# Kernel tuning notes

Measured on AMD Instinct MI355X. Metric: run time of the kernel, lower is better.

The kernel has to match this reference:

```python
import jax, jax.numpy as jnp
import numpy as np

BATCH, SEQ, HIDDEN = 2, 4096, 4096
HEADS, HEAD_DIM, BLOCK = 32, 128, 256
LAYER_IDX, N_LAYERS = 1, 32
EPS = 1e-5


def setup_inputs() -> dict:
    key = jax.random.key(0)
    ks = jax.random.split(key, 5)
    s = 0.02
    return {
        "hidden_states": jax.random.normal(ks[0], (BATCH, SEQ, HIDDEN), jnp.float32),
        "qkv_w": jax.random.normal(ks[1], (3 * HEADS * HEAD_DIM, HIDDEN), jnp.float32) * s,
        "out_w": jax.random.normal(ks[2], (HIDDEN, HEADS * HEAD_DIM), jnp.float32) * s,
        "gate_w": jax.random.normal(ks[3], (HEADS * HEAD_DIM, HIDDEN), jnp.float32) * s,
        "norm_w": jnp.ones((HEADS * HEAD_DIM,), jnp.float32),
    }


def _decays():
    # slope_rate: (h,1,1)
    base = 1.0 / 2.0 ** (8.0 / HEADS)
    exponent = jnp.arange(HEADS, dtype=jnp.float32) + 1.0
    factor = 1.0 - LAYER_IDX / (N_LAYERS - 1 + 1e-5) + 1e-5
    slope = (base ** exponent * factor)[:, None, None]
    r = jnp.arange(BLOCK, dtype=jnp.float32) + 1.0
    q_decay = jnp.exp(-slope * r[:, None])                 # (h, block, 1)
    k_decay = jnp.exp(-slope * (BLOCK - r)[:, None])       # (h, block, 1)
    diff = r[:, None] - r[None, :]                         # (block, block): i - j
    diag = slope[None] * diff[None, None]                  # (1, h, block, block)
    diag = jnp.where(diag >= 0, -diag, -jnp.inf)
    diag_decay = jnp.exp(diag)                             # causal intra-block decay
    block_decay = jnp.exp(-slope * BLOCK)                  # (h,1,1)
    return q_decay, k_decay, diag_decay, block_decay


def reference(hidden_states, qkv_w, out_w, gate_w, norm_w):
    b, s, _ = hidden_states.shape
    h, d, bs = HEADS, HEAD_DIM, BLOCK
    nb = s // bs
    q_decay, k_decay, diag_decay, block_decay = _decays()

    # qkv projection + silu, split per-head into q,k,v
    qkv = jax.nn.silu(hidden_states @ qkv_w.T)             # (b,s,3hd)
    qkv = qkv.reshape(b, s, h, 3, d)
    q = jnp.moveaxis(qkv[:, :, :, 0], 2, 1)                # (b,h,s,d)
    k = jnp.moveaxis(qkv[:, :, :, 1], 2, 1)
    v = jnp.moveaxis(qkv[:, :, :, 2], 2, 1)

    # split sequence into blocks, scan leading axis = block index
    def to_blocks(x):
        return jnp.moveaxis(x.reshape(b, h, nb, bs, d), 2, 0)  # (nb,b,h,bs,d)

    qb, kb, vb = to_blocks(q), to_blocks(k), to_blocks(v)

    def step(kv, blk):
        cq, ck, cv = blk
        # intra-block quadratic attention with causal decay
        scores = jnp.einsum('bhnd,bhmd->bhnm', cq, ck) * diag_decay
        intra = jnp.einsum('bhnm,bhmd->bhnd', scores, cv)
        # inter-block via decayed recurrent state kv: (b,h,d,d)
        inter = jnp.einsum('bhnd,bhde->bhne', cq * q_decay, kv)
        kv_next = kv * block_decay + jnp.einsum('bhnd,bhne->bhde', ck * k_decay, cv)
        return kv_next, intra + inter

    kv0 = jnp.zeros((b, h, d, d), hidden_states.dtype)
    _, out_blocks = jax.lax.scan(step, kv0, (qb, kb, vb))  # (nb,b,h,bs,d)

    attn = jnp.moveaxis(out_blocks, 0, 2)                  # (b,h,nb,bs,d)
    attn = attn.reshape(b, h, s, d).transpose(0, 2, 1, 3).reshape(b, s, h * d)

    # RMSNorm (fp32 accumulation, as MixtralRMSNorm)
    xf = attn.astype(jnp.float32)
    xf = xf * jax.lax.rsqrt(jnp.mean(xf * xf, axis=-1, keepdims=True) + EPS)
    normed = norm_w * xf.astype(attn.dtype)

    gate = jax.nn.sigmoid(hidden_states @ gate_w.T)
    return (gate * normed) @ out_w.T
```

## Files before the change

kernel.cpp:

```cpp
#include <hip/hip_runtime.h>

typedef unsigned short u16;
typedef __attribute__((ext_vector_type(4))) float f32x4;
typedef __attribute__((ext_vector_type(8))) __bf16 bf16x8;

#define SEQ   4096
#define HID   4096
#define HID3  12288

__device__ __forceinline__ float bf2f(u16 u){
  union { unsigned int i; float f; } v; v.i = ((unsigned int)u) << 16; return v.f;
}
__device__ __forceinline__ u16 f2bf(float f){
  union { float f; unsigned int i; } v; v.f = f;
  unsigned int r = (v.i + 0x7FFFu + ((v.i >> 16) & 1u)) >> 16;
  return (u16)r;
}
__device__ __forceinline__ float slope_of(int h){
  const float factor = 1.0f - 1.0f/(31.0f + 1e-5f) + 1e-5f;
  return exp2f(-0.25f * (float)(h + 1)) * factor;
}
__device__ __forceinline__ bf16x8 ld_bf8(const u16* p){
  return __builtin_bit_cast(bf16x8, *(const uint4*)p);
}
__device__ __forceinline__ void gload_lds16(const u16* g, u16* l){
  __builtin_amdgcn_global_load_lds((const __attribute__((address_space(1))) void*)g,
                                   (__attribute__((address_space(3))) void*)l, 16, 0, 0);
}

#define CVT_B0 33554432L
#define CVT_B1 83886080L
#define CVT_B2 100663296L
#define CVT_B3 117440512L
__global__ __launch_bounds__(256) void cvt4_kernel(const float* __restrict__ s0,
                                                   const float* __restrict__ s1,
                                                   const float* __restrict__ s2,
                                                   const float* __restrict__ s3,
                                                   u16* __restrict__ dst){
  long i = ((long)blockIdx.x * 256 + threadIdx.x) * 4;
  long stride = (long)gridDim.x * 1024;
  for (; i < CVT_B3; i += stride){
    const float* src;
    long off;
    if (i < CVT_B0){ src = s0; off = i; }
    else if (i < CVT_B1){ src = s1; off = i - CVT_B0; }
    else if (i < CVT_B2){ src = s2; off = i - CVT_B1; }
    else { src = s3; off = i - CVT_B2; }
    float4 v = *(const float4*)(src + off);
    ushort4 o;
    o.x = f2bf(v.x); o.y = f2bf(v.y); o.z = f2bf(v.z); o.w = f2bf(v.w);
    *(ushort4*)(dst + i) = o;
  }
}

template<int EPI>
__global__ __launch_bounds__(512) void gemm256(
    const u16* __restrict__ A, const u16* __restrict__ B, void* __restrict__ C,
    const u16* __restrict__ Aux, const float* __restrict__ Rs,
    const float* __restrict__ Nw, int M, int N, int K)
{
  __shared__ u16 ring[5][16384];
  const int t = threadIdx.x;
  const int w = t >> 6, l = t & 63, lr = l & 15, lk = l >> 4;
  const int mw = w >> 2, nw = w & 3;
  const int nbn = N >> 8;
  int nwg = gridDim.x;
  int bid = blockIdx.x;
  int bswz = (bid & 7) * (nwg >> 3) + (bid >> 3);
  int bm = bswz / nbn, bn = bswz % nbn;
  const u16* Abase = A + (long)(bm * 256) * K;
  const u16* Bbase = B + (long)(bn * 256) * K;
  const int NT = K >> 6;

  int sr[2], sku[2];
#pragma unroll
  for (int i = 0; i < 2; ++i){
    int dr = i * 64 + (t >> 3);
    int ul = (t & 7) ^ (dr & 7);
    sr[i]  = 2 * dr + (ul >> 2);
    sku[i] = ul & 3;
  }
  int offA[8], offB[4];
#pragma unroll
  for (int fn = 0; fn < 8; ++fn){
    int row = mw * 128 + fn * 16 + lr;
    offA[fn] = (row >> 1) * 64 + (((((row & 1) << 2) + lk) ^ ((row >> 1) & 7)) << 3);
  }
#pragma unroll
  for (int fe = 0; fe < 4; ++fe){
    int row = nw * 64 + fe * 16 + lr;
    offB[fe] = (row >> 1) * 64 + (((((row & 1) << 2) + lk) ^ ((row >> 1) & 7)) << 3);
  }

  auto stageA = [&](int kt, int c, int slot, int i){
    gload_lds16(Abase + (long)sr[i] * K + kt * 64 + c * 32 + sku[i] * 8,
                &ring[slot][i * 4096 + w * 512]);
  };
  auto stageB = [&](int kt, int c, int slot, int i){
    gload_lds16(Bbase + (long)sr[i] * K + kt * 64 + c * 32 + sku[i] * 8,
                &ring[slot][8192 + i * 4096 + w * 512]);
  };

  f32x4 acc[8][4] = {};

  stageA(0,0,0,0); stageA(0,0,0,1); stageB(0,0,0,0); stageB(0,0,0,1);
  stageA(0,1,1,0); stageA(0,1,1,1); stageB(0,1,1,0); stageB(0,1,1,1);
  if (1 < NT){ stageA(1,0,2,0); stageA(1,0,2,1); stageB(1,0,2,0); stageB(1,0,2,1); }
  asm volatile("s_waitcnt vmcnt(4)" ::: "memory");
  __builtin_amdgcn_s_barrier();

  int sa = 0;
  for (int p = 0; p < NT; ++p){
    int sb = sa + 1; if (sb >= 5) sb -= 5;
    int sx = sa + 3; if (sx >= 5) sx -= 5;
    int sy = sa + 4; if (sy >= 5) sy -= 5;
    const u16* Aa = &ring[sa][0];
    const u16* Ab = &ring[sb][0];
    const u16* Ba = &ring[sa][8192];
    const u16* Bb = &ring[sb][8192];
    bf16x8 bh0[4], bh1[4], afc0[8], afc1[8];

#pragma unroll
    for (int fe = 0; fe < 4; ++fe) bh0[fe] = ld_bf8(Ba + offB[fe]);
#pragma unroll
    for (int fn = 0; fn < 4; ++fn) afc0[fn] = ld_bf8(Aa + offA[fn]);
#pragma unroll
    for (int fn = 4; fn < 8; ++fn) afc0[fn] = ld_bf8(Aa + offA[fn]);
    if (p + 1 < NT){ stageA(p+1, 1, sx, 0); stageA(p+1, 1, sx, 1); }
    asm volatile("s_waitcnt lgkmcnt(4)" ::: "memory");
    __builtin_amdgcn_sched_barrier(0);
    __builtin_amdgcn_s_setprio(1);
#pragma unroll
    for (int fn = 0; fn < 4; ++fn)
#pragma unroll
      for (int fe = 0; fe < 4; ++fe)
        acc[fn][fe] = __builtin_amdgcn_mfma_f32_16x16x32_bf16(afc0[fn], bh0[fe], acc[fn][fe], 0, 0, 0);
    __builtin_amdgcn_s_setprio(0);

#pragma unroll
    for (int fe = 0; fe < 4; ++fe) bh1[fe] = ld_bf8(Bb + offB[fe]);
#pragma unroll
    for (int fn = 0; fn < 4; ++fn) afc1[fn] = ld_bf8(Ab + offA[fn]);
    if (p + 1 < NT){ stageB(p+1, 1, sx, 0); stageB(p+1, 1, sx, 1); }
    asm volatile("s_waitcnt lgkmcnt(8)" ::: "memory");
    __builtin_amdgcn_sched_barrier(0);
    __builtin_amdgcn_s_setprio(1);
#pragma unroll
    for (int fn = 4; fn < 8; ++fn)
#pragma unroll
      for (int fe = 0; fe < 4; ++fe)
        acc[fn][fe] = __builtin_amdgcn_mfma_f32_16x16x32_bf16(afc0[fn], bh0[fe], acc[fn][fe], 0, 0, 0);
    __builtin_amdgcn_s_setprio(0);

#pragma unroll
    for (int fn = 4; fn < 8; ++fn) afc1[fn] = ld_bf8(Ab + offA[fn]);
    if (p + 2 < NT){ stageA(p+2, 0, sy, 0); stageA(p+2, 0, sy, 1); }
    asm volatile("s_waitcnt lgkmcnt(4)" ::: "memory");
    __builtin_amdgcn_sched_barrier(0);
    __builtin_amdgcn_s_setprio(1);
#pragma unroll
    for (int fn = 0; fn < 4; ++fn)
#pragma unroll
      for (int fe = 0; fe < 4; ++fe)
        acc[fn][fe] = __builtin_amdgcn_mfma_f32_16x16x32_bf16(afc1[fn], bh1[fe], acc[fn][fe], 0, 0, 0);
    __builtin_amdgcn_s_setprio(0);

    if (p + 2 < NT){ stageB(p+2, 0, sy, 0); stageB(p+2, 0, sy, 1); }
    asm volatile("s_waitcnt lgkmcnt(0)" ::: "memory");
    __builtin_amdgcn_sched_barrier(0);
    __builtin_amdgcn_s_setprio(1);
#pragma unroll
    for (int fn = 4; fn < 8; ++fn)
#pragma unroll
      for (int fe = 0; fe < 4; ++fe)
        acc[fn][fe] = __builtin_amdgcn_mfma_f32_16x16x32_bf16(afc1[fn], bh1[fe], acc[fn][fe], 0, 0, 0);
    __builtin_amdgcn_s_setprio(0);

    if (p + 2 < NT) asm volatile("s_waitcnt vmcnt(4)" ::: "memory");
    else            asm volatile("s_waitcnt vmcnt(0)" ::: "memory");
    __builtin_amdgcn_s_barrier();
    sa += 2; if (sa >= 5) sa -= 5;
  }

  long crow = (long)bm * 256 + mw * 128 + lk * 4;
  long ccol = (long)bn * 256 + nw * 64 + lr;
#pragma unroll
  for (int fn = 0; fn < 8; ++fn)
#pragma unroll
    for (int fe = 0; fe < 4; ++fe)
#pragma unroll
      for (int reg = 0; reg < 4; ++reg){
        long row = crow + fn * 16 + reg;
        long col = ccol + fe * 16;
        float x = acc[fn][fe][reg];
        if (EPI == 0){
          ((u16*)C)[row * N + col] = f2bf(x / (1.0f + __expf(-x)));
        } else if (EPI == 1){
          float g = 1.0f / (1.0f + __expf(-x));
          float a = bf2f(Aux[row * N + col]);
          ((u16*)C)[row * N + col] = f2bf(g * a * Rs[row] * Nw[col]);
        } else {
          ((float*)C)[row * N + col] = x;
        }
      }
}

__global__ __launch_bounds__(256) void attn_contrib(
    const u16* __restrict__ qkv, float* __restrict__ ct)
{
  __shared__ u16 VT[128 * 258];
  __shared__ u16 KT[128 * 258];
  int wg = blockIdx.x;
  int bh = wg >> 4, blk = wg & 15;
  int b = bh >> 5, h = bh & 31;
  int t = threadIdx.x;
  float slope = slope_of(h);
  const u16* kg = qkv + ((long)(b * SEQ + blk * 256)) * HID3 + h * 384 + 128;
  const u16* vg = kg + 128;
#pragma unroll
  for (int i = 0; i < 16; ++i){
    int chunk = t + i * 256;
    int row = chunk >> 4, c8 = (chunk & 15) << 3;
    float kd = __expf(-slope * (float)(255 - row));
    uint4 kk = *(const uint4*)&kg[(long)row * HID3 + c8];
    uint4 vv = *(const uint4*)&vg[(long)row * HID3 + c8];
    const u16* ks = (const u16*)&kk;
    const u16* vs = (const u16*)&vv;
#pragma unroll
    for (int x = 0; x < 8; ++x){
      KT[(c8 + x) * 258 + row] = f2bf(bf2f(ks[x]) * kd);
      VT[(c8 + x) * 258 + row] = vs[x];
    }
  }
  __syncthreads();
  int w = t >> 6, l = t & 63, lr = l & 15, lk = l >> 4;
  int we = (w >> 1) * 64, wd = (w & 1) * 64;
  f32x4 acc[4][4] = {};
  for (int nc = 0; nc < 8; ++nc){
    bf16x8 va[4], kb[4];
#pragma unroll
    for (int f = 0; f < 4; ++f) va[f] = ld_bf8(&VT[(we + f * 16 + lr) * 258 + nc * 32 + lk * 8]);
#pragma unroll
    for (int f = 0; f < 4; ++f) kb[f] = ld_bf8(&KT[(wd + f * 16 + lr) * 258 + nc * 32 + lk * 8]);
#pragma unroll
    for (int fe = 0; fe < 4; ++fe)
#pragma unroll
      for (int fd = 0; fd < 4; ++fd)
        acc[fe][fd] = __builtin_amdgcn_mfma_f32_16x16x32_bf16(va[fe], kb[fd], acc[fe][fd], 0, 0, 0);
  }
  float* out = ct + (long)wg * 16384;
#pragma unroll
  for (int fe = 0; fe < 4; ++fe)
#pragma unroll
    for (int fd = 0; fd < 4; ++fd)
#pragma unroll
      for (int reg = 0; reg < 4; ++reg){
        int e = we + fe * 16 + lk * 4 + reg;
        int d = wd + fd * 16 + lr;
        out[e * 128 + d] = acc[fe][fd][reg];
      }
}

__global__ __launch_bounds__(256) void attn_scan(const float* __restrict__ ct,
                                                 u16* __restrict__ stTb)
{
  int g = blockIdx.x;
  int bh = g >> 2, sl = g & 3;
  int t = threadIdx.x;
  float bdec = __expf(-slope_of(bh & 31) * 256.0f);
  float cur[16];
#pragma unroll
  for (int i = 0; i < 16; ++i) cur[i] = 0.f;
  const float* base = ct + (long)bh * 16 * 16384 + sl * 4096;
  u16* ob = stTb + (long)bh * 16 * 16384 + sl * 4096;
  for (int blkI = 0; blkI < 16; ++blkI){
    const float* p = base + (long)blkI * 16384;
    u16* o = ob + (long)blkI * 16384;
#pragma unroll
    for (int i = 0; i < 16; ++i){
      o[t + i * 256] = f2bf(cur[i]);
      cur[i] = cur[i] * bdec + p[t + i * 256];
    }
  }
}

__global__ __launch_bounds__(512) void attn_mfma(
    const u16* __restrict__ qkv, const u16* __restrict__ stTb, u16* __restrict__ attn)
{
  __shared__ u16 Ks[256 * 130];
  __shared__ u16 VTs[128 * 258];
  __shared__ u16 Ps[4][64 * 34];
  int wg = blockIdx.x;
  int bh = wg >> 4, blk = wg & 15;
  int b = bh >> 5, h = bh & 31;
  int t = threadIdx.x;
  int w = t >> 6, l = t & 63, lr = l & 15, lk = l >> 4;
  int r = w >> 1, c = w & 1;
  float slope = slope_of(h);
  const u16* qg = qkv + ((long)(b * SEQ + blk * 256)) * HID3 + h * 384;
  const u16* kg = qg + 128;
  const u16* vg = qg + 256;

#pragma unroll
  for (int i = 0; i < 8; ++i){
    int chunk = t + i * 512;
    int row = chunk >> 4, c8 = (chunk & 15) << 3;
    *(uint4*)&Ks[row * 130 + c8] = *(const uint4*)&kg[(long)row * HID3 + c8];
    uint4 vv = *(const uint4*)&vg[(long)row * HID3 + c8];
    const u16* vs = (const u16*)&vv;
#pragma unroll
    for (int x = 0; x < 8; ++x) VTs[(c8 + x) * 258 + row] = vs[x];
  }
  bf16x8 qa[4][4];
#pragma unroll
  for (int fn = 0; fn < 4; ++fn)
#pragma unroll
    for (int kc = 0; kc < 4; ++kc)
      qa[fn][kc] = ld_bf8(&qg[(long)(r * 64 + fn * 16 + lr) * HID3 + kc * 32 + lk * 8]);
  f32x4 acc[4][4] = {};
  __syncthreads();

  int mtmax = 2 * r + 1;
  for (int mt = 0; mt < 8; ++mt){
    if (mt <= mtmax){
      f32x4 S[4] = {};
      int mrow = mt * 32 + c * 16 + lr;
      bf16x8 kb[4];
#pragma unroll
      for (int kc = 0; kc < 4; ++kc)
        kb[kc] = ld_bf8(&Ks[mrow * 130 + kc * 32 + lk * 8]);
#pragma unroll
      for (int fn = 0; fn < 4; ++fn)
#pragma unroll
        for (int kc = 0; kc < 4; ++kc)
          S[fn] = __builtin_amdgcn_mfma_f32_16x16x32_bf16(qa[fn][kc], kb[kc], S[fn], 0, 0, 0);
      int m = mt * 32 + c * 16 + lr;
#pragma unroll
      for (int fn = 0; fn < 4; ++fn)
#pragma unroll
        for (int reg = 0; reg < 4; ++reg){
          int n = r * 64 + fn * 16 + lk * 4 + reg;
          float dv = (n >= m) ? __expf(-slope * (float)(n - m)) : 0.f;
          Ps[r][(fn * 16 + lk * 4 + reg) * 34 + c * 16 + lr] = f2bf(S[fn][reg] * dv);
        }
    }
    __syncthreads();
    if (mt <= mtmax){
      bf16x8 pa[4], vb[4];
#pragma unroll
      for (int fn = 0; fn < 4; ++fn)
        pa[fn] = ld_bf8(&Ps[r][(fn * 16 + lr) * 34 + lk * 8]);
#pragma unroll
      for (int fe = 0; fe < 4; ++fe)
        vb[fe] = ld_bf8(&VTs[(c * 64 + fe * 16 + lr) * 258 + mt * 32 + lk * 8]);
#pragma unroll
      for (int fn = 0; fn < 4; ++fn)
#pragma unroll
        for (int fe = 0; fe < 4; ++fe)
          acc[fn][fe] = __builtin_amdgcn_mfma_f32_16x16x32_bf16(pa[fn], vb[fe], acc[fn][fe], 0, 0, 0);
    }
    __syncthreads();
  }

#pragma unroll
  for (int fn = 0; fn < 4; ++fn){
    int n = r * 64 + fn * 16 + lr;
    float qd = __expf(-slope * (float)(n + 1));
#pragma unroll
    for (int kc = 0; kc < 4; ++kc){
      union { bf16x8 v; u16 u[8]; } uu; uu.v = qa[fn][kc];
#pragma unroll
      for (int x = 0; x < 8; ++x) uu.u[x] = f2bf(bf2f(uu.u[x]) * qd);
      qa[fn][kc] = uu.v;
    }
  }
  const u16* sg = stTb + (long)(bh * 16 + blk) * 16384;
#pragma unroll
  for (int kc = 0; kc < 4; ++kc){
    bf16x8 sb2[4];
#pragma unroll
    for (int fe = 0; fe < 4; ++fe)
      sb2[fe] = ld_bf8(&sg[(c * 64 + fe * 16 + lr) * 128 + kc * 32 + lk * 8]);
#pragma unroll
    for (int fn = 0; fn < 4; ++fn)
#pragma unroll
      for (int fe = 0; fe < 4; ++fe)
        acc[fn][fe] = __builtin_amdgcn_mfma_f32_16x16x32_bf16(qa[fn][kc], sb2[fe], acc[fn][fe], 0, 0, 0);
  }

  u16* arow = attn + ((long)(b * SEQ + blk * 256)) * HID + h * 128;
#pragma unroll
  for (int fn = 0; fn < 4; ++fn)
#pragma unroll
    for (int fe = 0; fe < 4; ++fe)
#pragma unroll
      for (int reg = 0; reg < 4; ++reg){
        int n = r * 64 + fn * 16 + lk * 4 + reg;
        int col = c * 64 + fe * 16 + lr;
        arow[(long)n * HID + col] = f2bf(acc[fn][fe][reg]);
      }
}

__global__ __launch_bounds__(256) void rmsnorm_stats(const u16* __restrict__ attn,
                                                     float* __restrict__ rs)
{
  __shared__ float wsum[4];
  int row = blockIdx.x, t = threadIdx.x;
  const u16* p = attn + (long)row * HID;
  uint4 v0 = *(const uint4*)&p[t * 8];
  uint4 v1 = *(const uint4*)&p[t * 8 + 2048];
  const u16* a0 = (const u16*)&v0;
  const u16* a1 = (const u16*)&v1;
  float ss = 0.f;
#pragma unroll
  for (int x = 0; x < 8; ++x){
    float f0 = bf2f(a0[x]), f1 = bf2f(a1[x]);
    ss += f0 * f0 + f1 * f1;
  }
#pragma unroll
  for (int off = 32; off > 0; off >>= 1) ss += __shfl_down(ss, off);
  if ((t & 63) == 0) wsum[t >> 6] = ss;
  __syncthreads();
  if (t == 0)
    rs[row] = rsqrtf((wsum[0] + wsum[1] + wsum[2] + wsum[3]) * (1.0f / 4096.0f) + 1e-5f);
}

extern "C" void kernel_launch(void* const* d_in, const int* in_sizes, int n_in,
                              void* d_out, int out_size, void* d_ws, size_t ws_size,
                              hipStream_t stream)
{
  const float* hidden = (const float*)d_in[0];
  const float* qkv_w  = (const float*)d_in[1];
  const float* out_w  = (const float*)d_in[2];
  const float* gate_w = (const float*)d_in[3];
  const float* norm_w = (const float*)d_in[4];
  char* ws = (char*)d_ws;
  const long SZ_X  = 67108864L;
  const long SZ_WQ = 100663296L;
  const long SZ_WG = 33554432L;
  const long SZ_WO = 33554432L;
  const long SZ_QA = 201326592L;
  const long SZ_AT = 67108864L;
  u16* Xb   = (u16*)(ws);
  u16* Wq   = (u16*)(ws + SZ_X);
  u16* Wg   = (u16*)(ws + SZ_X + SZ_WQ);
  u16* Wo   = (u16*)(ws + SZ_X + SZ_WQ + SZ_WG);
  u16* qact = (u16*)(ws + SZ_X + SZ_WQ + SZ_WG + SZ_WO);
  u16* attn = (u16*)(ws + SZ_X + SZ_WQ + SZ_WG + SZ_WO + SZ_QA);
  float* st   = (float*)Wq;
  u16*   stTb = (u16*)(ws + SZ_X + 67108864L);
  float* rsbuf = (float*)Wq;
  u16* gated = qact;
  if (ws_size < (size_t)(SZ_X + SZ_WQ + SZ_WG + SZ_WO + SZ_QA + SZ_AT)) return;

  cvt4_kernel<<<2048, 256, 0, stream>>>(hidden, qkv_w, gate_w, out_w, Xb);

  gemm256<0><<<32 * 48, 512, 0, stream>>>(Xb, Wq, (void*)qact, nullptr, nullptr, nullptr,
                                          8192, 12288, 4096);

  attn_contrib<<<1024, 256, 0, stream>>>(qact, st);
  attn_scan<<<256, 256, 0, stream>>>(st, stTb);
  attn_mfma<<<1024, 512, 0, stream>>>(qact, stTb, attn);
  rmsnorm_stats<<<8192, 256, 0, stream>>>(attn, rsbuf);

  gemm256<1><<<32 * 16, 512, 0, stream>>>(Xb, Wg, (void*)gated, attn, rsbuf, norm_w,
                                          8192, 4096, 4096);
  gemm256<2><<<32 * 16, 512, 0, stream>>>(gated, Wo, d_out, nullptr, nullptr, nullptr,
                                          8192, 4096, 4096);
}
```

Baseline: 1.572 ms.

## Fuse RMSNorm sum-of-squares into attention epilogue and reorder GEMM tile mapping

The attention kernel now computes per-row partial sums of squares from its fp32 accumulators and writes them to a small buffer. A tiny finalize kernel reduces these 64 partials per row into the rsqrt scale. This replaces a pass that reread the whole bf16 attention tensor. The GEMM block mapping is also changed to iterate M-major instead of N-major, which alters L2 reuse of the weight and activation tiles. The stats now come from unrounded fp32 values instead of the bf16-rounded ones, a small numeric difference.

```diff
diff --git a/kernel.cpp b/kernel.cpp
--- a/kernel.cpp
+++ b/kernel.cpp
@@ -63,11 +63,11 @@
   const int t = threadIdx.x;
   const int w = t >> 6, l = t & 63, lr = l & 15, lk = l >> 4;
   const int mw = w >> 2, nw = w & 3;
-  const int nbn = N >> 8;
+  const int nbm = M >> 8;
   int nwg = gridDim.x;
   int bid = blockIdx.x;
   int bswz = (bid & 7) * (nwg >> 3) + (bid >> 3);
-  int bm = bswz / nbn, bn = bswz % nbn;
+  int bm = bswz % nbm, bn = bswz / nbm;
   const u16* Abase = A + (long)(bm * 256) * K;
   const u16* Bbase = B + (long)(bn * 256) * K;
   const int NT = K >> 6;
@@ -285,7 +285,8 @@
 }
 
 __global__ __launch_bounds__(512) void attn_mfma(
-    const u16* __restrict__ qkv, const u16* __restrict__ stTb, u16* __restrict__ attn)
+    const u16* __restrict__ qkv, const u16* __restrict__ stTb, u16* __restrict__ attn,
+    float* __restrict__ pss)
 {
   __shared__ u16 Ks[256 * 130];
   __shared__ u16 VTs[128 * 258];
@@ -389,40 +390,43 @@
   }
 
   u16* arow = attn + ((long)(b * SEQ + blk * 256)) * HID + h * 128;
+  long rowbase = (long)(b * SEQ + blk * 256 + r * 64);
 #pragma unroll
   for (int fn = 0; fn < 4; ++fn)
 #pragma unroll
-    for (int fe = 0; fe < 4; ++fe)
-#pragma unroll
-      for (int reg = 0; reg < 4; ++reg){
+    for (int reg = 0; reg < 4; ++reg){
+      float ss = 0.f;
+#pragma unroll
+      for (int fe = 0; fe < 4; ++fe){
         int n = r * 64 + fn * 16 + lk * 4 + reg;
         int col = c * 64 + fe * 16 + lr;
-        arow[(long)n * HID + col] = f2bf(acc[fn][fe][reg]);
+        float x = acc[fn][fe][reg];
+        arow[(long)n * HID + col] = f2bf(x);
+        ss += x * x;
       }
-}
-
-__global__ __launch_bounds__(256) void rmsnorm_stats(const u16* __restrict__ attn,
-                                                     float* __restrict__ rs)
-{
-  __shared__ float wsum[4];
-  int row = blockIdx.x, t = threadIdx.x;
-  const u16* p = attn + (long)row * HID;
-  uint4 v0 = *(const uint4*)&p[t * 8];
-  uint4 v1 = *(const uint4*)&p[t * 8 + 2048];
-  const u16* a0 = (const u16*)&v0;
-  const u16* a1 = (const u16*)&v1;
-  float ss = 0.f;
-#pragma unroll
-  for (int x = 0; x < 8; ++x){
-    float f0 = bf2f(a0[x]), f1 = bf2f(a1[x]);
-    ss += f0 * f0 + f1 * f1;
-  }
-#pragma unroll
-  for (int off = 32; off > 0; off >>= 1) ss += __shfl_down(ss, off);
-  if ((t & 63) == 0) wsum[t >> 6] = ss;
-  __syncthreads();
-  if (t == 0)
-    rs[row] = rsqrtf((wsum[0] + wsum[1] + wsum[2] + wsum[3]) * (1.0f / 4096.0f) + 1e-5f);
+      ss += __shfl_xor(ss, 1);
+      ss += __shfl_xor(ss, 2);
+      ss += __shfl_xor(ss, 4);
+      ss += __shfl_xor(ss, 8);
+      if (lr == 0){
+        int nloc = fn * 16 + lk * 4 + reg;
+        pss[(rowbase + nloc) * 64 + h * 2 + c] = ss;
+      }
+    }
+}
+
+__global__ __launch_bounds__(256) void rms_finalize(const float* __restrict__ pss,
+                                                    float* __restrict__ rs)
+{
+  int row = blockIdx.x * 256 + threadIdx.x;
+  const float* p = pss + (long)row * 64;
+  float s = 0.f;
+#pragma unroll
+  for (int i = 0; i < 64; i += 4){
+    float4 v = *(const float4*)(p + i);
+    s += v.x + v.y + v.z + v.w;
+  }
+  rs[row] = rsqrtf(s * (1.0f / 4096.0f) + 1e-5f);
 }
 
 extern "C" void kernel_launch(void* const* d_in, const int* in_sizes, int n_in,
@@ -449,7 +453,8 @@
   u16* attn = (u16*)(ws + SZ_X + SZ_WQ + SZ_WG + SZ_WO + SZ_QA);
   float* st   = (float*)Wq;
   u16*   stTb = (u16*)(ws + SZ_X + 67108864L);
-  float* rsbuf = (float*)Wq;
+  float* pss   = (float*)Wq;
+  float* rsbuf = (float*)(ws + SZ_X + 4194304L);
   u16* gated = qact;
   if (ws_size < (size_t)(SZ_X + SZ_WQ + SZ_WG + SZ_WO + SZ_QA + SZ_AT)) return;
 
@@ -460,8 +465,8 @@
 
   attn_contrib<<<1024, 256, 0, stream>>>(qact, st);
   attn_scan<<<256, 256, 0, stream>>>(st, stTb);
-  attn_mfma<<<1024, 512, 0, stream>>>(qact, stTb, attn);
-  rmsnorm_stats<<<8192, 256, 0, stream>>>(attn, rsbuf);
+  attn_mfma<<<1024, 512, 0, stream>>>(qact, stTb, attn, pss);
+  rms_finalize<<<32, 256, 0, stream>>>(pss, rsbuf);
 
   gemm256<1><<<32 * 16, 512, 0, stream>>>(Xb, Wg, (void*)gated, attn, rsbuf, norm_w,
                                           8192, 4096, 4096);
```

Measured after the change: 1.619 ms. +3.0%, slower.

## Pre-pack GEMM operands into swizzled tile-contiguous layout during bf16 conversion

Applied to the files above, without the earlier changes.

The fp32-to-bf16 conversion kernel now writes operands in a pre-tiled, pre-swizzled layout: each 256-row by 32-column chunk becomes one contiguous 16 KB block matching the LDS ring layout. The GEMM staging loads then read fully contiguous 16-byte segments per thread instead of strided rows. The gate GEMM epilogue writes its output in the same packed layout so the output-projection GEMM can consume it directly. The intent is more coalesced global-to-LDS loads in all three GEMMs. In exchange, the conversion kernel's stores are scattered and its reads are strided, and the epilogue needs extra index arithmetic.

```diff
diff --git a/kernel.cpp b/kernel.cpp
--- a/kernel.cpp
+++ b/kernel.cpp
@@ -28,28 +28,33 @@
                                    (__attribute__((address_space(3))) void*)l, 16, 0, 0);
 }
 
-#define CVT_B0 33554432L
-#define CVT_B1 83886080L
-#define CVT_B2 100663296L
-#define CVT_B3 117440512L
-__global__ __launch_bounds__(256) void cvt4_kernel(const float* __restrict__ s0,
-                                                   const float* __restrict__ s1,
-                                                   const float* __restrict__ s2,
-                                                   const float* __restrict__ s3,
-                                                   u16* __restrict__ dst){
-  long i = ((long)blockIdx.x * 256 + threadIdx.x) * 4;
-  long stride = (long)gridDim.x * 1024;
-  for (; i < CVT_B3; i += stride){
-    const float* src;
-    long off;
-    if (i < CVT_B0){ src = s0; off = i; }
-    else if (i < CVT_B1){ src = s1; off = i - CVT_B0; }
-    else if (i < CVT_B2){ src = s2; off = i - CVT_B1; }
-    else { src = s3; off = i - CVT_B2; }
-    float4 v = *(const float4*)(src + off);
-    ushort4 o;
-    o.x = f2bf(v.x); o.y = f2bf(v.y); o.z = f2bf(v.z); o.w = f2bf(v.w);
-    *(ushort4*)(dst + i) = o;
+__global__ __launch_bounds__(256) void cvt4p_kernel(const float* __restrict__ s0,
+                                                    const float* __restrict__ s1,
+                                                    const float* __restrict__ s2,
+                                                    const float* __restrict__ s3,
+                                                    u16* __restrict__ dst){
+  int c = blockIdx.x;
+  int tr = c >> 7, kch = c & 127;
+  const float* src; int rowbase;
+  if (tr < 32){ src = s0; rowbase = tr * 256; }
+  else if (tr < 80){ src = s1; rowbase = (tr - 32) * 256; }
+  else if (tr < 96){ src = s2; rowbase = (tr - 80) * 256; }
+  else { src = s3; rowbase = (tr - 96) * 256; }
+  u16* out = dst + (long)c * 8192;
+#pragma unroll
+  for (int pass = 0; pass < 4; ++pass){
+    int q = pass * 256 + threadIdx.x;
+    int dr = q >> 3, up = q & 7;
+    int ul = up ^ (dr & 7);
+    int row = 2 * dr + (ul >> 2);
+    int k8 = ul & 3;
+    const float* sp = src + (long)(rowbase + row) * 4096 + kch * 32 + k8 * 8;
+    float4 v0 = *(const float4*)sp;
+    float4 v1 = *(const float4*)(sp + 4);
+    ushort4 o0 = { f2bf(v0.x), f2bf(v0.y), f2bf(v0.z), f2bf(v0.w) };
+    ushort4 o1 = { f2bf(v1.x), f2bf(v1.y), f2bf(v1.z), f2bf(v1.w) };
+    *(ushort4*)(out + q * 8) = o0;
+    *(ushort4*)(out + q * 8 + 4) = o1;
   }
 }
 
@@ -64,22 +69,13 @@
   const int w = t >> 6, l = t & 63, lr = l & 15, lk = l >> 4;
   const int mw = w >> 2, nw = w & 3;
   const int nbn = N >> 8;
+  const int nkc = K >> 5;
   int nwg = gridDim.x;
   int bid = blockIdx.x;
   int bswz = (bid & 7) * (nwg >> 3) + (bid >> 3);
   int bm = bswz / nbn, bn = bswz % nbn;
-  const u16* Abase = A + (long)(bm * 256) * K;
-  const u16* Bbase = B + (long)(bn * 256) * K;
   const int NT = K >> 6;
 
-  int sr[2], sku[2];
-#pragma unroll
-  for (int i = 0; i < 2; ++i){
-    int dr = i * 64 + (t >> 3);
-    int ul = (t & 7) ^ (dr & 7);
-    sr[i]  = 2 * dr + (ul >> 2);
-    sku[i] = ul & 3;
-  }
   int offA[8], offB[4];
 #pragma unroll
   for (int fn = 0; fn < 8; ++fn){
@@ -93,11 +89,11 @@
   }
 
   auto stageA = [&](int kt, int c, int slot, int i){
-    gload_lds16(Abase + (long)sr[i] * K + kt * 64 + c * 32 + sku[i] * 8,
+    gload_lds16(A + ((long)bm * nkc + kt * 2 + c) * 8192 + i * 4096 + t * 8,
                 &ring[slot][i * 4096 + w * 512]);
   };
   auto stageB = [&](int kt, int c, int slot, int i){
-    gload_lds16(Bbase + (long)sr[i] * K + kt * 64 + c * 32 + sku[i] * 8,
+    gload_lds16(B + ((long)bn * nkc + kt * 2 + c) * 8192 + i * 4096 + t * 8,
                 &ring[slot][8192 + i * 4096 + w * 512]);
   };
 
@@ -198,7 +194,12 @@
         } else if (EPI == 1){
           float g = 1.0f / (1.0f + __expf(-x));
           float a = bf2f(Aux[row * N + col]);
-          ((u16*)C)[row * N + col] = f2bf(g * a * Rs[row] * Nw[col]);
+          int r256 = (int)row & 255;
+          int dr2 = r256 >> 1;
+          int ul2 = ((r256 & 1) << 2) | (((int)col & 31) >> 3);
+          int u2 = ul2 ^ (dr2 & 7);
+          long idx = ((long)(row >> 8) * 128 + (col >> 5)) * 8192 + dr2 * 64 + u2 * 8 + (col & 7);
+          ((u16*)C)[idx] = f2bf(g * a * Rs[row] * Nw[col]);
         } else {
           ((float*)C)[row * N + col] = x;
         }
@@ -453,7 +454,7 @@
   u16* gated = qact;
   if (ws_size < (size_t)(SZ_X + SZ_WQ + SZ_WG + SZ_WO + SZ_QA + SZ_AT)) return;
 
-  cvt4_kernel<<<2048, 256, 0, stream>>>(hidden, qkv_w, gate_w, out_w, Xb);
+  cvt4p_kernel<<<14336, 256, 0, stream>>>(hidden, qkv_w, gate_w, out_w, Xb);
 
   gemm256<0><<<32 * 48, 512, 0, stream>>>(Xb, Wq, (void*)qact, nullptr, nullptr, nullptr,
                                           8192, 12288, 4096);
```

Result: faster. 1.529 ms (median of 2 runs) (-2.7%).
